# Optimization experiments

Measured on AMD Instinct MI355X. Metric: run time of the kernel, lower is better.

Reference implementation:

```python
import jax, jax.numpy as jnp
import numpy as np

H = 1024
V = 50257
S = 8192


def setup_inputs() -> dict:
    key = jax.random.key(0)
    ks = jax.random.split(key, 13)
    s = 0.02  # param init scale
    return {
        "input": jax.random.randint(ks[0], (1,), 0, V),
        "hidden": jax.random.normal(ks[1], (1, 1, H), jnp.float32),
        "encoder_outputs": jax.random.normal(ks[2], (S, H), jnp.float32),
        "embedding": jax.random.normal(ks[3], (V, H), jnp.float32) * s,
        "attn_w": jax.random.normal(ks[4], (1, 2 * H), jnp.float32) * s,
        "attn_b": jnp.zeros((1,), jnp.float32),
        "comb_w": jax.random.normal(ks[5], (H, 2 * H), jnp.float32) * s,
        "comb_b": jnp.zeros((H,), jnp.float32),
        "w_ih": jax.random.normal(ks[6], (3 * H, H), jnp.float32) * s,
        "w_hh": jax.random.normal(ks[7], (3 * H, H), jnp.float32) * s,
        "b_ih": jnp.zeros((3 * H,), jnp.float32),
        "b_hh": jnp.zeros((3 * H,), jnp.float32),
        "out_w": jax.random.normal(ks[8], (V, H), jnp.float32) * s,
        "out_b": jnp.zeros((V,), jnp.float32),
    }


def reference(input, hidden, encoder_outputs, embedding, attn_w, attn_b,
              comb_w, comb_b, w_ih, w_hh, b_ih, b_hh, out_w, out_b):
    # embedded = embedding(input).view(1,1,-1); dropout in eval mode = identity
    emb = embedding[input[0]]            # [H]
    h0 = hidden[0, 0]                    # [H]
    # Original loop computes the SAME score attn(cat(emb, hidden)) for every
    # timestep -> softmax over a constant vector (uniform weights). Compute the
    # scalar once and broadcast (same math, one GEMV instead of S launches).
    score = jnp.concatenate([emb, h0]) @ attn_w[0] + attn_b[0]   # scalar
    seq_len = encoder_outputs.shape[0]
    attn_weights = jax.nn.softmax(jnp.broadcast_to(score, (seq_len,)))  # [S]
    attn_applied = attn_weights @ encoder_outputs                # [H]
    combined = jnp.concatenate([emb, attn_applied]) @ comb_w.T + comb_b  # [H]
    x = jax.nn.relu(combined)
    # Single GRU step (torch nn.GRU gate math)
    gi = w_ih @ x + b_ih                 # [3H]
    gh = w_hh @ h0 + b_hh                # [3H]
    i_r, i_z, i_n = jnp.split(gi, 3)
    h_r, h_z, h_n = jnp.split(gh, 3)
    r = jax.nn.sigmoid(i_r + h_r)
    z = jax.nn.sigmoid(i_z + h_z)
    n = jnp.tanh(i_n + r * h_n)
    h_new = (1.0 - z) * n + z * h0       # [H]
    logits = h_new @ out_w.T + out_b     # [V]
    output = jax.nn.log_softmax(logits)[None, :]   # [1, V]
    return output, h_new[None, None, :], attn_weights[None, :]
```

## Files before the change

kernel.cpp:

```cpp
#include <hip/hip_runtime.h>
#include <math.h>

#define HN 1024
#define VN 50257
#define SN 8192

#define WS_PARTIAL 0
#define WS_AA      262144
#define WS_X       263168
#define WS_GH      264192
#define WS_CEMB    267264
#define WS_HNEW    270336
#define WS_LOGITS  271360
#define WS_EXPD    321618

__device__ __forceinline__ float wred(float v) {
#pragma unroll
  for (int m = 32; m; m >>= 1) v += __shfl_xor(v, m);
  return v;
}

__device__ __forceinline__ float dot4(float4 a, float4 b) {
  return a.x * b.x + a.y * b.y + a.z * b.z + a.w * b.w;
}

__global__ __launch_bounds__(1024) void k1_front(
    const float* __restrict__ enc, const float* __restrict__ w_hh,
    const float* __restrict__ hidden, const int* __restrict__ token,
    const float* __restrict__ embedding, const float* __restrict__ comb_w,
    const float* __restrict__ comb_b, float* __restrict__ ws,
    float* __restrict__ out_attn) {
  const int blk = blockIdx.x, t = threadIdx.x;
  __shared__ float4 lds[1024];
  {
    const int g = t >> 8, c4 = t & 255;
    const float4* e4 = (const float4*)enc + ((size_t)blk * 32 + g * 8) * 256 + c4;
    float4 acc = make_float4(0.f, 0.f, 0.f, 0.f);
#pragma unroll
    for (int r = 0; r < 8; ++r) {
      float4 v = e4[r * 256];
      acc.x += v.x; acc.y += v.y; acc.z += v.z; acc.w += v.w;
    }
    lds[t] = acc;
  }
  __syncthreads();
  if (t < 256) {
    float4 a = lds[t], b = lds[t + 256], c = lds[t + 512], d = lds[t + 768];
    float4 s = make_float4(a.x + b.x + c.x + d.x, a.y + b.y + c.y + d.y,
                           a.z + b.z + c.z + d.z, a.w + b.w + c.w + d.w);
    ((float4*)(ws + WS_PARTIAL))[blk * 256 + t] = s;
  }
  if (t < 32) out_attn[blk * 32 + t] = 1.f / 8192.f;
  const int w = t >> 6, l = t & 63;
  if (w < 12) {
    const int r = blk * 12 + w;
    const float4* h4 = (const float4*)hidden;
    const float4* m4 = (const float4*)w_hh + (size_t)r * 256;
    float acc = dot4(m4[l], h4[l]) + dot4(m4[64 + l], h4[64 + l]) +
                dot4(m4[128 + l], h4[128 + l]) + dot4(m4[192 + l], h4[192 + l]);
    acc = wred(acc);
    if (l == 0) ws[WS_GH + r] = acc;
  } else {
    const int i = blk * 4 + (w - 12);
    const int tok = token[0];
    const float4* emb4 = (const float4*)embedding + (size_t)tok * 256;
    const float4* cw4 = (const float4*)comb_w + (size_t)i * 512;
    float acc = dot4(cw4[l], emb4[l]) + dot4(cw4[64 + l], emb4[64 + l]) +
                dot4(cw4[128 + l], emb4[128 + l]) + dot4(cw4[192 + l], emb4[192 + l]);
    acc = wred(acc);
    if (l == 0) ws[WS_CEMB + i] = acc + comb_b[i];
  }
}

__global__ __launch_bounds__(1024) void k2_reduce(float* __restrict__ ws) {
  __shared__ float lds[1024];
  const int t = threadIdx.x, b = blockIdx.x;
  const int c = b * 32 + (t & 31), rg = t >> 5;
  const float* p = ws + WS_PARTIAL;
  float s = 0.f;
#pragma unroll
  for (int j = 0; j < 8; ++j) s += p[(rg * 8 + j) * 1024 + c];
  lds[t] = s;
  __syncthreads();
  if (t < 32) {
    float a = 0.f;
#pragma unroll
    for (int j = 0; j < 32; ++j) a += lds[j * 32 + t];
    ws[WS_AA + b * 32 + t] = a * (1.f / 8192.f);
  }
}

__global__ void k3_x(const float* __restrict__ comb_w, float* __restrict__ ws) {
  const int w = threadIdx.x >> 6, l = threadIdx.x & 63;
  const int i = blockIdx.x * 4 + w;
  const float4* aa4 = (const float4*)(ws + WS_AA);
  const float4* cw4 = (const float4*)comb_w + (size_t)i * 512 + 256;
  float acc = dot4(cw4[l], aa4[l]) + dot4(cw4[64 + l], aa4[64 + l]) +
              dot4(cw4[128 + l], aa4[128 + l]) + dot4(cw4[192 + l], aa4[192 + l]);
  acc = wred(acc);
  if (l == 0) ws[WS_X + i] = fmaxf(ws[WS_CEMB + i] + acc, 0.f);
}

__global__ void k4_gates_h(const float* __restrict__ w_ih,
                           const float* __restrict__ b_ih, const float* __restrict__ b_hh,
                           const float* __restrict__ hidden, float* __restrict__ ws,
                           float* __restrict__ d_out) {
  const int w = threadIdx.x >> 6, l = threadIdx.x & 63;
  const int i = blockIdx.x * 4 + w;
  const float4* x4 = (const float4*)(ws + WS_X);
  float4 xv0 = x4[l], xv1 = x4[64 + l], xv2 = x4[128 + l], xv3 = x4[192 + l];
  const float4* m0 = (const float4*)w_ih + (size_t)i * 256;
  const float4* m1 = (const float4*)w_ih + (size_t)(i + 1024) * 256;
  const float4* m2 = (const float4*)w_ih + (size_t)(i + 2048) * 256;
  float a0 = dot4(m0[l], xv0) + dot4(m0[64 + l], xv1) +
             dot4(m0[128 + l], xv2) + dot4(m0[192 + l], xv3);
  float a1 = dot4(m1[l], xv0) + dot4(m1[64 + l], xv1) +
             dot4(m1[128 + l], xv2) + dot4(m1[192 + l], xv3);
  float a2 = dot4(m2[l], xv0) + dot4(m2[64 + l], xv1) +
             dot4(m2[128 + l], xv2) + dot4(m2[192 + l], xv3);
  a0 = wred(a0); a1 = wred(a1); a2 = wred(a2);
  if (l == 0) {
    float ir = a0 + b_ih[i];
    float iz = a1 + b_ih[i + 1024];
    float inn = a2 + b_ih[i + 2048];
    float hr = ws[WS_GH + i] + b_hh[i];
    float hz = ws[WS_GH + i + 1024] + b_hh[i + 1024];
    float hn = ws[WS_GH + i + 2048] + b_hh[i + 2048];
    float rg = 1.f / (1.f + expf(-(ir + hr)));
    float zg = 1.f / (1.f + expf(-(iz + hz)));
    float ng = tanhf(inn + rg * hn);
    float h = (1.f - zg) * ng + zg * hidden[i];
    ws[WS_HNEW + i] = h;
    d_out[VN + i] = h;
  }
}

__global__ void k5_logits(const float* __restrict__ out_w, const float* __restrict__ out_b,
                          float* __restrict__ ws) {
  const int blk = blockIdx.x, t = threadIdx.x;
  const int w = t >> 6, l = t & 63;
  const int gw = blk * 4 + w;
  const float4* h4p = (const float4*)(ws + WS_HNEW);
  float4 h0_ = h4p[l], h1_ = h4p[64 + l], h2_ = h4p[128 + l], h3_ = h4p[192 + l];
  const float4* ow4 = (const float4*)out_w;
  double eacc = 0.0;
  {
    const int v0 = gw, v1 = gw + 8448, v2 = gw + 16896;
    const float4* r0 = ow4 + (size_t)v0 * 256;
    const float4* r1 = ow4 + (size_t)v1 * 256;
    const float4* r2 = ow4 + (size_t)v2 * 256;
    float a0 = dot4(r0[l], h0_) + dot4(r0[64 + l], h1_) +
               dot4(r0[128 + l], h2_) + dot4(r0[192 + l], h3_);
    float a1 = dot4(r1[l], h0_) + dot4(r1[64 + l], h1_) +
               dot4(r1[128 + l], h2_) + dot4(r1[192 + l], h3_);
    float a2 = dot4(r2[l], h0_) + dot4(r2[64 + l], h1_) +
               dot4(r2[128 + l], h2_) + dot4(r2[192 + l], h3_);
    a0 = wred(a0); a1 = wred(a1); a2 = wred(a2);
    if (l == 0) {
      float lg0 = a0 + out_b[v0];
      float lg1 = a1 + out_b[v1];
      float lg2 = a2 + out_b[v2];
      ws[WS_LOGITS + v0] = lg0;
      ws[WS_LOGITS + v1] = lg1;
      ws[WS_LOGITS + v2] = lg2;
      eacc += (double)expf(lg0) + (double)expf(lg1) + (double)expf(lg2);
    }
  }
  {
    const int v0 = gw + 25344, v1 = gw + 33792, v2 = gw + 42240;
    const bool ok2 = (v2 < VN);
    const float4* r0 = ow4 + (size_t)v0 * 256;
    const float4* r1 = ow4 + (size_t)v1 * 256;
    const float4* r2 = ow4 + (size_t)(ok2 ? v2 : v1) * 256;
    float a0 = dot4(r0[l], h0_) + dot4(r0[64 + l], h1_) +
               dot4(r0[128 + l], h2_) + dot4(r0[192 + l], h3_);
    float a1 = dot4(r1[l], h0_) + dot4(r1[64 + l], h1_) +
               dot4(r1[128 + l], h2_) + dot4(r1[192 + l], h3_);
    float a2 = dot4(r2[l], h0_) + dot4(r2[64 + l], h1_) +
               dot4(r2[128 + l], h2_) + dot4(r2[192 + l], h3_);
    a0 = wred(a0); a1 = wred(a1); a2 = wred(a2);
    if (l == 0) {
      float lg0 = a0 + out_b[v0];
      float lg1 = a1 + out_b[v1];
      ws[WS_LOGITS + v0] = lg0;
      ws[WS_LOGITS + v1] = lg1;
      eacc += (double)expf(lg0) + (double)expf(lg1);
      if (ok2) {
        float lg2 = a2 + out_b[v2];
        ws[WS_LOGITS + v2] = lg2;
        eacc += (double)expf(lg2);
      }
    }
  }
  __shared__ double sd[4];
  if (l == 0) sd[w] = eacc;
  __syncthreads();
  if (t == 0) ((double*)(ws + WS_EXPD))[blk] = sd[0] + sd[1] + sd[2] + sd[3];
}

__global__ void k6_final(const float* __restrict__ ws, float* __restrict__ d_out) {
  __shared__ double sd[256];
  const int t = threadIdx.x;
  const double* ed = (const double*)(ws + WS_EXPD);
  double a = 0.0;
#pragma unroll
  for (int j = 0; j < 8; ++j) a += ed[t + j * 256];
  if (t < 64) a += ed[t + 2048];
  sd[t] = a;
  __syncthreads();
  for (int s = 128; s; s >>= 1) {
    if (t < s) sd[t] += sd[t + s];
    __syncthreads();
  }
  const float logZ = (float)log(sd[0]);
  const int v = blockIdx.x * 256 + t;
  if (v < VN) d_out[v] = ws[WS_LOGITS + v] - logZ;
}

extern "C" void kernel_launch(void* const* d_in, const int* in_sizes, int n_in,
                              void* d_out, int out_size, void* d_ws, size_t ws_size,
                              hipStream_t stream) {
  const int* token = (const int*)d_in[0];
  const float* hidden = (const float*)d_in[1];
  const float* enc = (const float*)d_in[2];
  const float* embedding = (const float*)d_in[3];
  const float* comb_w = (const float*)d_in[6];
  const float* comb_b = (const float*)d_in[7];
  const float* w_ih = (const float*)d_in[8];
  const float* w_hh = (const float*)d_in[9];
  const float* b_ih = (const float*)d_in[10];
  const float* b_hh = (const float*)d_in[11];
  const float* out_w = (const float*)d_in[12];
  const float* out_b = (const float*)d_in[13];
  float* out = (float*)d_out;
  float* ws = (float*)d_ws;

  k1_front<<<256, 1024, 0, stream>>>(enc, w_hh, hidden, token, embedding,
                                     comb_w, comb_b, ws, out + VN + HN);
  k2_reduce<<<32, 1024, 0, stream>>>(ws);
  k3_x<<<256, 256, 0, stream>>>(comb_w, ws);
  k4_gates_h<<<256, 256, 0, stream>>>(w_ih, b_ih, b_hh, hidden, ws, out);
  k5_logits<<<2112, 256, 0, stream>>>(out_w, out_b, ws);
  k6_final<<<197, 256, 0, stream>>>(ws, out);
}
```

Baseline: 58.16 us.

## Restructure encoder column-sum to cut partials and fuse reduce into attention GEMV

The encoder column reduction now has each block sum a 1024-row chunk over a 32-column stripe, so only 8 partial rows go to workspace instead of 256. This removes the separate reduce kernel. A new mid kernel does the w_hh GEMV and, in its other blocks, finishes the 8-way partial sum into shared memory before the attended comb_w GEMV. That merges two launches into one, trading a launch and a 1 MB partial buffer round-trip for redundant per-block partial summation. The encoder reads are now 128-byte scalar stripes rather than full float4 rows, which may lower coalescing efficiency.

```diff
diff --git a/kernel.cpp b/kernel.cpp
--- a/kernel.cpp
+++ b/kernel.cpp
@@ -6,13 +6,12 @@
 #define SN 8192
 
 #define WS_PARTIAL 0
-#define WS_AA      262144
-#define WS_X       263168
-#define WS_GH      264192
-#define WS_CEMB    267264
-#define WS_HNEW    270336
-#define WS_LOGITS  271360
-#define WS_EXPD    321618
+#define WS_X       8192
+#define WS_GH      9216
+#define WS_CEMB    12288
+#define WS_HNEW    13312
+#define WS_LOGITS  14336
+#define WS_EXPD    64594
 
 __device__ __forceinline__ float wred(float v) {
 #pragma unroll
@@ -25,35 +24,49 @@
 }
 
 __global__ __launch_bounds__(1024) void k1_front(
-    const float* __restrict__ enc, const float* __restrict__ w_hh,
-    const float* __restrict__ hidden, const int* __restrict__ token,
+    const float* __restrict__ enc, const int* __restrict__ token,
     const float* __restrict__ embedding, const float* __restrict__ comb_w,
     const float* __restrict__ comb_b, float* __restrict__ ws,
     float* __restrict__ out_attn) {
   const int blk = blockIdx.x, t = threadIdx.x;
-  __shared__ float4 lds[1024];
+  __shared__ float lds[1024];
+  const int chunk = blk >> 5, stripe = blk & 31;
   {
-    const int g = t >> 8, c4 = t & 255;
-    const float4* e4 = (const float4*)enc + ((size_t)blk * 32 + g * 8) * 256 + c4;
-    float4 acc = make_float4(0.f, 0.f, 0.f, 0.f);
-#pragma unroll
-    for (int r = 0; r < 8; ++r) {
-      float4 v = e4[r * 256];
-      acc.x += v.x; acc.y += v.y; acc.z += v.z; acc.w += v.w;
-    }
-    lds[t] = acc;
+    const float* base =
+        enc + ((size_t)chunk * 1024 + (t >> 5)) * 1024 + stripe * 32 + (t & 31);
+    float s = 0.f;
+#pragma unroll 8
+    for (int j = 0; j < 32; ++j) s += base[j * 32768];
+    lds[t] = s;
   }
   __syncthreads();
-  if (t < 256) {
-    float4 a = lds[t], b = lds[t + 256], c = lds[t + 512], d = lds[t + 768];
-    float4 s = make_float4(a.x + b.x + c.x + d.x, a.y + b.y + c.y + d.y,
-                           a.z + b.z + c.z + d.z, a.w + b.w + c.w + d.w);
-    ((float4*)(ws + WS_PARTIAL))[blk * 256 + t] = s;
-  }
-  if (t < 32) out_attn[blk * 32 + t] = 1.f / 8192.f;
+  if (t < 32) {
+    float a = 0.f;
+#pragma unroll
+    for (int j = 0; j < 32; ++j) a += lds[t + j * 32];
+    ws[WS_PARTIAL + chunk * 1024 + stripe * 32 + t] = a;
+    out_attn[blk * 32 + t] = 1.f / 8192.f;
+  }
   const int w = t >> 6, l = t & 63;
-  if (w < 12) {
-    const int r = blk * 12 + w;
+  if (w < 4) {
+    const int i = blk * 4 + w;
+    const int tok = token[0];
+    const float4* emb4 = (const float4*)embedding + (size_t)tok * 256;
+    const float4* cw4 = (const float4*)comb_w + (size_t)i * 512;
+    float acc = dot4(cw4[l], emb4[l]) + dot4(cw4[64 + l], emb4[64 + l]) +
+                dot4(cw4[128 + l], emb4[128 + l]) + dot4(cw4[192 + l], emb4[192 + l]);
+    acc = wred(acc);
+    if (l == 0) ws[WS_CEMB + i] = acc + comb_b[i];
+  }
+}
+
+__global__ __launch_bounds__(1024) void k2_mid(
+    const float* __restrict__ w_hh, const float* __restrict__ hidden,
+    const float* __restrict__ comb_w, float* __restrict__ ws) {
+  const int blk = blockIdx.x, t = threadIdx.x;
+  const int w = t >> 6, l = t & 63;
+  if (blk < 192) {
+    const int r = blk * 16 + w;
     const float4* h4 = (const float4*)hidden;
     const float4* m4 = (const float4*)w_hh + (size_t)r * 256;
     float acc = dot4(m4[l], h4[l]) + dot4(m4[64 + l], h4[64 + l]) +
@@ -61,44 +74,20 @@
     acc = wred(acc);
     if (l == 0) ws[WS_GH + r] = acc;
   } else {
-    const int i = blk * 4 + (w - 12);
-    const int tok = token[0];
-    const float4* emb4 = (const float4*)embedding + (size_t)tok * 256;
-    const float4* cw4 = (const float4*)comb_w + (size_t)i * 512;
-    float acc = dot4(cw4[l], emb4[l]) + dot4(cw4[64 + l], emb4[64 + l]) +
-                dot4(cw4[128 + l], emb4[128 + l]) + dot4(cw4[192 + l], emb4[192 + l]);
+    __shared__ float aas[1024];
+    float s = 0.f;
+#pragma unroll
+    for (int j = 0; j < 8; ++j) s += ws[WS_PARTIAL + j * 1024 + t];
+    aas[t] = s * (1.f / 8192.f);
+    __syncthreads();
+    const int i = (blk - 192) * 16 + w;
+    const float4* aa4 = (const float4*)aas;
+    const float4* cw4 = (const float4*)comb_w + (size_t)i * 512 + 256;
+    float acc = dot4(cw4[l], aa4[l]) + dot4(cw4[64 + l], aa4[64 + l]) +
+                dot4(cw4[128 + l], aa4[128 + l]) + dot4(cw4[192 + l], aa4[192 + l]);
     acc = wred(acc);
-    if (l == 0) ws[WS_CEMB + i] = acc + comb_b[i];
-  }
-}
-
-__global__ __launch_bounds__(1024) void k2_reduce(float* __restrict__ ws) {
-  __shared__ float lds[1024];
-  const int t = threadIdx.x, b = blockIdx.x;
-  const int c = b * 32 + (t & 31), rg = t >> 5;
-  const float* p = ws + WS_PARTIAL;
-  float s = 0.f;
-#pragma unroll
-  for (int j = 0; j < 8; ++j) s += p[(rg * 8 + j) * 1024 + c];
-  lds[t] = s;
-  __syncthreads();
-  if (t < 32) {
-    float a = 0.f;
-#pragma unroll
-    for (int j = 0; j < 32; ++j) a += lds[j * 32 + t];
-    ws[WS_AA + b * 32 + t] = a * (1.f / 8192.f);
-  }
-}
-
-__global__ void k3_x(const float* __restrict__ comb_w, float* __restrict__ ws) {
-  const int w = threadIdx.x >> 6, l = threadIdx.x & 63;
-  const int i = blockIdx.x * 4 + w;
-  const float4* aa4 = (const float4*)(ws + WS_AA);
-  const float4* cw4 = (const float4*)comb_w + (size_t)i * 512 + 256;
-  float acc = dot4(cw4[l], aa4[l]) + dot4(cw4[64 + l], aa4[64 + l]) +
-              dot4(cw4[128 + l], aa4[128 + l]) + dot4(cw4[192 + l], aa4[192 + l]);
-  acc = wred(acc);
-  if (l == 0) ws[WS_X + i] = fmaxf(ws[WS_CEMB + i] + acc, 0.f);
+    if (l == 0) ws[WS_X + i] = fmaxf(ws[WS_CEMB + i] + acc, 0.f);
+  }
 }
 
 __global__ void k4_gates_h(const float* __restrict__ w_ih,
@@ -235,10 +224,9 @@
   float* out = (float*)d_out;
   float* ws = (float*)d_ws;
 
-  k1_front<<<256, 1024, 0, stream>>>(enc, w_hh, hidden, token, embedding,
-                                     comb_w, comb_b, ws, out + VN + HN);
-  k2_reduce<<<32, 1024, 0, stream>>>(ws);
-  k3_x<<<256, 256, 0, stream>>>(comb_w, ws);
+  k1_front<<<256, 1024, 0, stream>>>(enc, token, embedding, comb_w, comb_b,
+                                     ws, out + VN + HN);
+  k2_mid<<<256, 1024, 0, stream>>>(w_hh, hidden, comb_w, ws);
   k4_gates_h<<<256, 256, 0, stream>>>(w_ih, b_ih, b_hh, hidden, ws, out);
   k5_logits<<<2112, 256, 0, stream>>>(out_w, out_b, ws);
   k6_final<<<197, 256, 0, stream>>>(ws, out);
```

Result: no change. 57.93 us (-0.4%).
